# Optimization experiments

Hardware: AMD Instinct MI355X
Metric: run time of the kernel (lower is better)

## Reference

```python
import jax, jax.numpy as jnp
import numpy as np

C = 1152            # hidden_size
HEADS_LA = 36       # LiteLA heads = hidden_size // 32
HEADS_X = 16        # cross-attention heads
HID = int(C * 2.5)  # GLUMBConv hidden = 2880
B, N, M = 2, 4096, 300
EPS_LA = 1e-8
EPS_LN = 1e-6


def _ln(x):
    # LayerNorm without affine (adaLN-single style)
    mu = jnp.mean(x, -1, keepdims=True)
    var = jnp.mean((x - mu) ** 2, -1, keepdims=True)
    return (x - mu) * jax.lax.rsqrt(var + EPS_LN)


def _lite_la(x, qkv_w, proj_w, proj_b):
    b, n, c = x.shape
    d = c // HEADS_LA
    qkv = x @ qkv_w.T                       # (B,N,3C)
    q, k, v = jnp.split(qkv, 3, -1)
    r = lambda t: t.transpose(0, 2, 1).reshape(b, HEADS_LA, d, n)
    q = jax.nn.relu(r(q))
    k = jax.nn.relu(r(k))
    v = r(v)
    # pad v with a row of ones (PAD_VAL=1) for the normalizer
    v = jnp.concatenate([v, jnp.ones((b, HEADS_LA, 1, n), v.dtype)], 2)  # (B,h,d+1,N)
    vk = jnp.einsum('bhdn,bhen->bhde', v, k)    # (B,h,d+1,d)
    out = jnp.einsum('bhde,bhen->bhdn', vk, q)  # (B,h,d+1,N)
    out = out[:, :, :-1] / (out[:, :, -1:] + EPS_LA)
    out = out.reshape(b, c, n).transpose(0, 2, 1)
    return out @ proj_w.T + proj_b


def _cross(x, y, q_w, q_b, kv_w, kv_b, pw, pb):
    b, n, c = x.shape
    d = c // HEADS_X
    q = (x @ q_w.T + q_b).reshape(b, n, HEADS_X, d).transpose(0, 2, 1, 3)
    k, v = jnp.split(y @ kv_w.T + kv_b, 2, -1)
    k = k.reshape(b, -1, HEADS_X, d).transpose(0, 2, 1, 3)
    v = v.reshape(b, -1, HEADS_X, d).transpose(0, 2, 1, 3)
    scale = float(1.0 / np.sqrt(d))
    a = jax.nn.softmax(jnp.einsum('bhnd,bhmd->bhnm', q, k) * scale, -1)
    o = jnp.einsum('bhnm,bhmd->bhnd', a, v).transpose(0, 2, 1, 3).reshape(b, n, c)
    return o @ pw.T + pb


def _glumb(x, inv_w, inv_b, dw_w, dw_b, pw_w):
    b, n, c = x.shape
    H = W = int(np.sqrt(n))
    h = jax.nn.silu(x @ inv_w.T + inv_b)          # 1x1 inverted conv + silu, (B,N,2*HID)
    h = h.transpose(0, 2, 1).reshape(b, 2 * HID, H, W)
    h = jax.lax.conv_general_dilated(
        h, dw_w, (1, 1), 'SAME',
        feature_group_count=2 * HID,
        dimension_numbers=('NCHW', 'OIHW', 'NCHW'))
    h = h + dw_b[None, :, None, None]
    a, g = jnp.split(h, 2, 1)
    h = a * jax.nn.silu(g)                         # GLU
    h = h.reshape(b, HID, n).transpose(0, 2, 1)
    return h @ pw_w.T                              # 1x1 point conv, no bias/act


def setup_inputs() -> dict:
    key = jax.random.key(0)
    ks = jax.random.split(key, 12)
    p = lambda k, shp: (0.02 * jax.random.normal(k, shp)).astype(jnp.float32)
    z = lambda shp: jnp.zeros(shp, jnp.float32)
    return dict(
        x=jax.random.normal(ks[0], (B, N, C), jnp.float32),
        y=jax.random.normal(ks[1], (B, M, C), jnp.float32),
        t=jax.random.normal(ks[2], (B, 6, C), jnp.float32),
        sst=p(ks[3], (6, C)),
        qkv_w=p(ks[4], (3 * C, C)),
        aproj_w=p(ks[5], (C, C)), aproj_b=z((C,)),
        q_w=p(ks[6], (C, C)), q_b=z((C,)),
        kv_w=p(ks[7], (2 * C, C)), kv_b=z((2 * C,)),
        cproj_w=p(ks[8], (C, C)), cproj_b=z((C,)),
        inv_w=p(ks[9], (2 * HID, C)), inv_b=z((2 * HID,)),
        dw_w=p(ks[10], (2 * HID, 1, 3, 3)), dw_b=z((2 * HID,)),
        pw_w=p(ks[11], (C, HID)),
    )


def reference(x, y, t, sst, qkv_w, aproj_w, aproj_b, q_w, q_b, kv_w, kv_b,
              cproj_w, cproj_b, inv_w, inv_b, dw_w, dw_b, pw_w):
    m = sst[None] + t  # (B,6,C)
    sh_a, sc_a, g_a, sh_m, sc_m, g_m = [m[:, i:i + 1] for i in range(6)]
    x = x + g_a * _lite_la(_ln(x) * (1 + sc_a) + sh_a, qkv_w, aproj_w, aproj_b)
    x = x + _cross(x, y, q_w, q_b, kv_w, kv_b, cproj_w, cproj_b)
    x = x + g_m * _glumb(_ln(x) * (1 + sc_m) + sh_m, inv_w, inv_b, dw_w, dw_b, pw_w)
    return x
```

## Files before the change

### kernel.cpp

```cpp
#include <hip/hip_runtime.h>
#include <hip/hip_bf16.h>
#include <cstdint>
#include <cstddef>

#define CD    1152
#define NTOK  4096
#define MTOK  300
#define BSZ   2
#define HID2  5760
#define HIDD  2880
#define ROWS  (BSZ*NTOK)
#define KVROWS (BSZ*MTOK)

using bf16 = __hip_bfloat16;
typedef __bf16 bf16x8 __attribute__((ext_vector_type(8)));
typedef float f32x4 __attribute__((ext_vector_type(4)));

__device__ __forceinline__ float b2f(bf16 h) { return __bfloat162float(h); }
__device__ __forceinline__ bf16  f2b(float f) { return __float2bfloat16(f); }
__device__ __forceinline__ bf16x8 bz8() {
    bf16x8 v;
    #pragma unroll
    for (int j = 0; j < 8; ++j) v[j] = (__bf16)0.0f;
    return v;
}

__device__ __forceinline__ void gload16(const void* g, void* l) {
    __builtin_amdgcn_global_load_lds(
        (const __attribute__((address_space(1))) void*)g,
        (__attribute__((address_space(3))) void*)l, 16, 0, 0);
}

__global__ void cast_bf(const float* __restrict__ in, bf16* __restrict__ o, int n) {
    int i = blockIdx.x * 256 + threadIdx.x;
    if (i < n) o[i] = f2b(in[i]);
}

__global__ void zero_f32(float* __restrict__ p, int n) {
    int i = blockIdx.x * 256 + threadIdx.x;
    if (i < n) p[i] = 0.f;
}

__global__ void add_mod(const float* __restrict__ sst, const float* __restrict__ t,
                        float* __restrict__ m, int n, int per) {
    int i = blockIdx.x * 256 + threadIdx.x;
    if (i < n) m[i] = sst[i % per] + t[i];
}

__global__ void prep_dww(const float* __restrict__ dww, bf16* __restrict__ wt) {
    int i = blockIdx.x * 256 + threadIdx.x;
    if (i < 9 * HID2) {
        const int k = i / HID2, c = i - k * HID2;
        wt[i] = f2b(dww[c * 9 + k]);
    }
}

__global__ __launch_bounds__(256) void ln_mod(
    const float* __restrict__ xf, const float* __restrict__ m,
    int shRow, int scRow, bf16* __restrict__ out) {
    const int row = blockIdx.x;
    const int b = row >> 12;
    float s = 0.f, s2 = 0.f;
    for (int c = threadIdx.x; c < CD; c += 256) {
        float v = xf[(size_t)row * CD + c];
        s += v; s2 += v * v;
    }
    #pragma unroll
    for (int off = 32; off; off >>= 1) {
        s  += __shfl_down(s,  off, 64);
        s2 += __shfl_down(s2, off, 64);
    }
    __shared__ float red[8];
    const int wid = threadIdx.x >> 6, lane = threadIdx.x & 63;
    if (lane == 0) { red[wid] = s; red[4 + wid] = s2; }
    __syncthreads();
    s  = red[0] + red[1] + red[2] + red[3];
    s2 = red[4] + red[5] + red[6] + red[7];
    const float mu  = s / CD;
    const float var = s2 / CD - mu * mu;
    const float rs  = rsqrtf(var + 1e-6f);
    const float* sh = &m[((size_t)b * 6 + shRow) * CD];
    const float* sc = &m[((size_t)b * 6 + scRow) * CD];
    for (int c = threadIdx.x; c < CD; c += 256) {
        float v = xf[(size_t)row * CD + c];
        out[(size_t)row * CD + c] = f2b((v - mu) * rs * (1.f + sc[c]) + sh[c]);
    }
}

template<int EPI>
__global__ __launch_bounds__(256) void gemm_bt(
    const bf16* __restrict__ A, const bf16* __restrict__ W,
    const float* __restrict__ bias, const float* __restrict__ resf,
    const float* __restrict__ gate, int gateStride,
    bf16* __restrict__ outb, float* __restrict__ outf,
    int rows, int K, int Nout, int reluCols) {
    __shared__ __align__(16) char smem[33792];
    bf16* As = (bf16*)smem;
    bf16* Bs = (bf16*)(smem + 16384);
    const int tid = threadIdx.x;
    const int row0 = blockIdx.x * 128;
    const int col0 = blockIdx.y * 128;
    const int wid = tid >> 6, lane = tid & 63;
    const int wm = wid & 1, wn = wid >> 1;
    const int l16 = lane & 15, l4 = lane >> 4;
    f32x4 acc[4][4] = {};

    const int sr = tid >> 3;
    const int kbsw = (((tid & 7) ^ (sr & 7)) << 3);
    int gra[4], gcl[4];
    #pragma unroll
    for (int p = 0; p < 4; ++p) {
        int r = row0 + p * 32 + sr; if (r >= rows) r = rows - 1;
        gra[p] = r;
        gcl[p] = col0 + p * 32 + sr;
    }
    char* AsB = smem + wid * 1024;
    char* BsB = smem + 16384 + wid * 1024;

    for (int k0 = 0; k0 < K; k0 += 64) {
        __syncthreads();
        #pragma unroll
        for (int p = 0; p < 4; ++p) {
            gload16(&A[(size_t)gra[p] * K + k0 + kbsw], AsB + p * 4096);
            gload16(&W[(size_t)gcl[p] * K + k0 + kbsw], BsB + p * 4096);
        }
        __syncthreads();
        #pragma unroll
        for (int kk = 0; kk < 2; ++kk) {
            bf16x8 a[4], b[4];
            #pragma unroll
            for (int i = 0; i < 4; ++i) {
                const int ar = wm * 64 + i * 16 + l16;
                a[i] = *(const bf16x8*)&As[ar * 64 + ((((kk << 2) + l4) ^ (ar & 7)) << 3)];
            }
            #pragma unroll
            for (int j = 0; j < 4; ++j) {
                const int br = wn * 64 + j * 16 + l16;
                b[j] = *(const bf16x8*)&Bs[br * 64 + ((((kk << 2) + l4) ^ (br & 7)) << 3)];
            }
            #pragma unroll
            for (int i = 0; i < 4; ++i)
                #pragma unroll
                for (int j = 0; j < 4; ++j)
                    acc[i][j] = __builtin_amdgcn_mfma_f32_16x16x32_bf16(a[i], b[j], acc[i][j], 0, 0, 0);
        }
    }

    float* Lf = (float*)smem;
    const int erow = tid >> 4;
    const int ecol = (tid & 15) * 8;
    const int gc = col0 + ecol;
    #pragma unroll
    for (int pass = 0; pass < 2; ++pass) {
        __syncthreads();
        if (wm == pass) {
            #pragma unroll
            for (int i = 0; i < 4; ++i)
                #pragma unroll
                for (int j = 0; j < 4; ++j) {
                    const int lc = wn * 64 + j * 16 + l16;
                    #pragma unroll
                    for (int r = 0; r < 4; ++r)
                        Lf[(i * 16 + l4 * 4 + r) * 130 + lc] = acc[i][j][r];
                }
        }
        __syncthreads();
        #pragma unroll
        for (int rr = 0; rr < 4; ++rr) {
            const int lrow = rr * 16 + erow;
            const int gr = row0 + pass * 64 + lrow;
            if (gr >= rows) continue;
            float v[8];
            #pragma unroll
            for (int c = 0; c < 8; ++c) v[c] = Lf[lrow * 130 + ecol + c];
            const size_t oi0 = (size_t)gr * Nout + gc;
            if (EPI == 0) {
                bf16x8 ob;
                #pragma unroll
                for (int c = 0; c < 8; ++c) ob[c] = (__bf16)(v[c] + bias[gc + c]);
                *(bf16x8*)&outb[oi0] = ob;
            } else if (EPI == 1) {
                bf16x8 ob;
                #pragma unroll
                for (int c = 0; c < 8; ++c) {
                    float t = v[c];
                    if (gc + c < reluCols) t = fmaxf(t, 0.0f);
                    ob[c] = (__bf16)t;
                }
                *(bf16x8*)&outb[oi0] = ob;
            } else if (EPI == 2) {
                bf16x8 ob;
                #pragma unroll
                for (int c = 0; c < 8; ++c) {
                    float t = v[c] + bias[gc + c];
                    t = t / (1.0f + __expf(-t));
                    ob[c] = (__bf16)t;
                }
                *(bf16x8*)&outb[oi0] = ob;
            } else if (EPI == 3) {
                const float* gp = &gate[(gr >> 12) * gateStride + gc];
                const float* rp = &resf[oi0];
                f32x4 o0, o1; bf16x8 ob;
                #pragma unroll
                for (int c = 0; c < 8; ++c) {
                    float t = v[c] + bias[gc + c];
                    t = rp[c] + gp[c] * t;
                    if (c < 4) o0[c] = t; else o1[c - 4] = t;
                    ob[c] = (__bf16)t;
                }
                *(f32x4*)&outf[oi0] = o0;
                *(f32x4*)&outf[oi0 + 4] = o1;
                *(bf16x8*)&outb[oi0] = ob;
            } else if (EPI == 4) {
                const float* rp = &resf[oi0];
                f32x4 o0, o1;
                #pragma unroll
                for (int c = 0; c < 8; ++c) {
                    float t = rp[c] + v[c] + bias[gc + c];
                    if (c < 4) o0[c] = t; else o1[c - 4] = t;
                }
                *(f32x4*)&outf[oi0] = o0;
                *(f32x4*)&outf[oi0 + 4] = o1;
            } else {
                const float* gp = &gate[(gr >> 12) * gateStride + gc];
                const float* rp = &resf[oi0];
                f32x4 o0, o1;
                #pragma unroll
                for (int c = 0; c < 8; ++c) {
                    float t = rp[c] + gp[c] * v[c];
                    if (c < 4) o0[c] = t; else o1[c - 4] = t;
                }
                *(f32x4*)&outf[oi0] = o0;
                *(f32x4*)&outf[oi0 + 4] = o1;
            }
        }
    }
}

__global__ __launch_bounds__(256) void lite_vk(
    const bf16* __restrict__ qkv, float* __restrict__ vk) {
    const int b = blockIdx.x / 36, h = blockIdx.x % 36;
    const int n0 = blockIdx.y * 256;
    __shared__ bf16 ksm[64 * 32];
    __shared__ bf16 vsm[64 * 32];
    const int t = threadIdx.x;
    const int ev = t >> 3, kq = (t & 7) * 4;
    float a0 = 0, a1 = 0, a2 = 0, a3 = 0;
    float q0 = 0, q1 = 0, q2 = 0, q3 = 0;
    for (int tile = 0; tile < 4; ++tile) {
        const int nb = n0 + tile * 64;
        __syncthreads();
        {
            const int nl = t >> 2, part = (t & 3) * 8;
            const size_t rbase = ((size_t)b * NTOK + nb + nl) * (3 * CD);
            *(bf16x8*)&ksm[nl * 32 + part] = *(const bf16x8*)&qkv[rbase + CD     + h * 32 + part];
            *(bf16x8*)&vsm[nl * 32 + part] = *(const bf16x8*)&qkv[rbase + 2 * CD + h * 32 + part];
        }
        __syncthreads();
        #pragma unroll 4
        for (int nl = 0; nl < 64; ++nl) {
            const float vv = b2f(vsm[nl * 32 + ev]);
            const float k0 = b2f(ksm[nl * 32 + kq + 0]);
            const float k1 = b2f(ksm[nl * 32 + kq + 1]);
            const float k2 = b2f(ksm[nl * 32 + kq + 2]);
            const float k3 = b2f(ksm[nl * 32 + kq + 3]);
            a0 += vv * k0; a1 += vv * k1; a2 += vv * k2; a3 += vv * k3;
            if (ev == 0) { q0 += k0; q1 += k1; q2 += k2; q3 += k3; }
        }
    }
    float* dst = &vk[(((size_t)b * 36 + h) * 33 + ev) * 32 + kq];
    atomicAdd(dst + 0, a0); atomicAdd(dst + 1, a1);
    atomicAdd(dst + 2, a2); atomicAdd(dst + 3, a3);
    if (ev == 0) {
        float* d2 = &vk[(((size_t)b * 36 + h) * 33 + 32) * 32 + kq];
        atomicAdd(d2 + 0, q0); atomicAdd(d2 + 1, q1);
        atomicAdd(d2 + 2, q2); atomicAdd(d2 + 3, q3);
    }
}

__global__ __launch_bounds__(256) void lite_out(
    const bf16* __restrict__ qkv, const float* __restrict__ vk,
    bf16* __restrict__ u) {
    const int b = blockIdx.x / 36, h = blockIdx.x % 36;
    const int n = blockIdx.y * 256 + threadIdx.x;
    __shared__ float vks[33 * 32];
    const float* src = &vk[((size_t)b * 36 + h) * 33 * 32];
    for (int i = threadIdx.x; i < 33 * 32; i += 256) vks[i] = src[i];
    __syncthreads();
    float q[32];
    const bf16* qp = &qkv[((size_t)b * NTOK + n) * (3 * CD) + h * 32];
    #pragma unroll
    for (int e = 0; e < 32; ++e) q[e] = b2f(qp[e]);
    float denom = 0.f;
    #pragma unroll
    for (int e = 0; e < 32; ++e) denom += vks[32 * 32 + e] * q[e];
    const float rd = 1.f / (denom + 1e-8f);
    bf16* up = &u[((size_t)b * NTOK + n) * CD + h * 32];
    #pragma unroll 1
    for (int d = 0; d < 32; ++d) {
        float acc = 0.f;
        #pragma unroll
        for (int e = 0; e < 32; ++e) acc += vks[d * 32 + e] * q[e];
        up[d] = f2b(acc * rd);
    }
}

__global__ __launch_bounds__(256) void cross_attn_mfma(
    const bf16* __restrict__ qx, const bf16* __restrict__ kvb,
    bf16* __restrict__ attn) {
    const int b = blockIdx.x >> 4, h = blockIdx.x & 15;
    const int row0 = blockIdx.y * 64;
    __shared__ bf16 Ks[320 * 72];
    __shared__ bf16 Vt[80 * 328];
    __shared__ bf16 Ps[64 * 328];
    const int tid = threadIdx.x;
    const int wid = tid >> 6, lane = tid & 63;
    const int l16 = lane & 15, l4 = lane >> 4;
    const bf16 zb = f2b(0.f);
    const bf16x8 zv8 = bz8();

    for (int i = tid; i < 80 * 328; i += 256) Vt[i] = zb;
    for (int idx = tid; idx < 320 * 9; idx += 256) {
        const int m = idx / 9, part = (idx % 9) * 8;
        if (m < MTOK)
            *(bf16x8*)&Ks[m * 72 + part] =
                *(const bf16x8*)&kvb[((size_t)b * MTOK + m) * (2 * CD) + h * 72 + part];
        else
            *(bf16x8*)&Ks[m * 72 + part] = zv8;
    }
    __syncthreads();
    for (int i = tid; i < MTOK * 72; i += 256) {
        const int m = i / 72, d = i - m * 72;
        Vt[d * 328 + m] = kvb[((size_t)b * MTOK + m) * (2 * CD) + CD + h * 72 + d];
    }
    for (int i = lane; i < 16 * 16; i += 64)
        Ps[(wid * 16 + (i >> 4)) * 328 + 304 + (i & 15)] = zb;

    bf16x8 aq[3];
    {
        const int qrow = row0 + wid * 16 + l16;
        const bf16* qp = &qx[((size_t)b * NTOK + qrow) * CD + h * 72];
        aq[0] = *(const bf16x8*)&qp[l4 * 8];
        aq[1] = *(const bf16x8*)&qp[32 + l4 * 8];
        aq[2] = (l4 == 0) ? *(const bf16x8*)&qp[64] : zv8;
    }

    f32x4 sa[19] = {};
    #pragma unroll
    for (int t = 0; t < 19; ++t) {
        const bf16* kr = &Ks[(t * 16 + l16) * 72];
        bf16x8 b0 = *(const bf16x8*)&kr[l4 * 8];
        bf16x8 b1 = *(const bf16x8*)&kr[32 + l4 * 8];
        bf16x8 b2 = (l4 == 0) ? *(const bf16x8*)&kr[64] : zv8;
        sa[t] = __builtin_amdgcn_mfma_f32_16x16x32_bf16(aq[0], b0, sa[t], 0, 0, 0);
        sa[t] = __builtin_amdgcn_mfma_f32_16x16x32_bf16(aq[1], b1, sa[t], 0, 0, 0);
        sa[t] = __builtin_amdgcn_mfma_f32_16x16x32_bf16(aq[2], b2, sa[t], 0, 0, 0);
    }

    const float scale = 0.11785113019775792f;
    if (l16 >= 12) { sa[18][0] = sa[18][1] = sa[18][2] = sa[18][3] = -3.0e37f; }
    float mr[4] = {-3.0e38f, -3.0e38f, -3.0e38f, -3.0e38f};
    #pragma unroll
    for (int t = 0; t < 19; ++t)
        #pragma unroll
        for (int r = 0; r < 4; ++r) {
            const float s = sa[t][r] * scale;
            sa[t][r] = s;
            mr[r] = fmaxf(mr[r], s);
        }
    #pragma unroll
    for (int off = 1; off < 16; off <<= 1)
        #pragma unroll
        for (int r = 0; r < 4; ++r)
            mr[r] = fmaxf(mr[r], __shfl_xor(mr[r], off, 64));
    float lr[4] = {0.f, 0.f, 0.f, 0.f};
    #pragma unroll
    for (int t = 0; t < 19; ++t)
        #pragma unroll
        for (int r = 0; r < 4; ++r) {
            const float p = __expf(sa[t][r] - mr[r]);
            lr[r] += p;
            Ps[(wid * 16 + l4 * 4 + r) * 328 + t * 16 + l16] = f2b(p);
        }
    #pragma unroll
    for (int off = 1; off < 16; off <<= 1)
        #pragma unroll
        for (int r = 0; r < 4; ++r)
            lr[r] += __shfl_xor(lr[r], off, 64);
    __syncthreads();

    f32x4 oa[5] = {};
    #pragma unroll
    for (int kc = 0; kc < 10; ++kc) {
        bf16x8 pa = *(const bf16x8*)&Ps[(wid * 16 + l16) * 328 + kc * 32 + l4 * 8];
        #pragma unroll
        for (int dt = 0; dt < 5; ++dt) {
            bf16x8 vb = *(const bf16x8*)&Vt[(dt * 16 + l16) * 328 + kc * 32 + l4 * 8];
            oa[dt] = __builtin_amdgcn_mfma_f32_16x16x32_bf16(pa, vb, oa[dt], 0, 0, 0);
        }
    }
    #pragma unroll
    for (int r = 0; r < 4; ++r) {
        const float rinv = 1.f / lr[r];
        const int gr = row0 + wid * 16 + l4 * 4 + r;
        bf16* op = &attn[((size_t)b * NTOK + gr) * CD + h * 72];
        #pragma unroll
        for (int dt = 0; dt < 5; ++dt) {
            const int d = dt * 16 + l16;
            if (d < 72) op[d] = f2b(oa[dt][r] * rinv);
        }
    }
}

__global__ __launch_bounds__(128) void dwconv_glu2(
    const bf16* __restrict__ hbuf, const bf16* __restrict__ wt,
    const float* __restrict__ dwb, bf16* __restrict__ glu) {
    const int cg = blockIdx.y * 128 + threadIdx.x;
    if (cg >= 360) return;
    const int c0 = cg * 8;
    const int n = blockIdx.x & 4095;
    const int b = blockIdx.x >> 12;
    const int y0 = n >> 6, x0 = n & 63;
    float a[8], g[8];
    #pragma unroll
    for (int j = 0; j < 8; ++j) { a[j] = dwb[c0 + j]; g[j] = dwb[HIDD + c0 + j]; }
    #pragma unroll
    for (int dy = -1; dy <= 1; ++dy) {
        const int yy = y0 + dy;
        if (yy < 0 || yy >= 64) continue;
        #pragma unroll
        for (int dx = -1; dx <= 1; ++dx) {
            const int xx = x0 + dx;
            if (xx < 0 || xx >= 64) continue;
            const int k = (dy + 1) * 3 + (dx + 1);
            const size_t base = ((size_t)b * NTOK + yy * 64 + xx) * HID2;
            const bf16x8 va = *(const bf16x8*)&hbuf[base + c0];
            const bf16x8 vg = *(const bf16x8*)&hbuf[base + HIDD + c0];
            const bf16x8 wa = *(const bf16x8*)&wt[k * HID2 + c0];
            const bf16x8 wg = *(const bf16x8*)&wt[k * HID2 + HIDD + c0];
            #pragma unroll
            for (int j = 0; j < 8; ++j) {
                a[j] += (float)wa[j] * (float)va[j];
                g[j] += (float)wg[j] * (float)vg[j];
            }
        }
    }
    bf16x8 o;
    #pragma unroll
    for (int j = 0; j < 8; ++j) {
        const float s = g[j] / (1.f + __expf(-g[j]));
        o[j] = (__bf16)(a[j] * s);
    }
    *(bf16x8*)&glu[((size_t)b * NTOK + n) * HIDD + c0] = o;
}

extern "C" void kernel_launch(void* const* d_in, const int* in_sizes, int n_in,
                              void* d_out, int out_size, void* d_ws, size_t ws_size,
                              hipStream_t stream) {
    (void)in_sizes; (void)n_in; (void)out_size; (void)ws_size;
    const float* x       = (const float*)d_in[0];
    const float* y       = (const float*)d_in[1];
    const float* t       = (const float*)d_in[2];
    const float* sst     = (const float*)d_in[3];
    const float* qkv_w   = (const float*)d_in[4];
    const float* aproj_w = (const float*)d_in[5];
    const float* aproj_b = (const float*)d_in[6];
    const float* q_w     = (const float*)d_in[7];
    const float* q_b     = (const float*)d_in[8];
    const float* kv_w    = (const float*)d_in[9];
    const float* kv_b    = (const float*)d_in[10];
    const float* cproj_w = (const float*)d_in[11];
    const float* cproj_b = (const float*)d_in[12];
    const float* inv_w   = (const float*)d_in[13];
    const float* inv_b   = (const float*)d_in[14];
    const float* dw_w    = (const float*)d_in[15];
    const float* dw_b    = (const float*)d_in[16];
    const float* pw_w    = (const float*)d_in[17];
    float* out = (float*)d_out;

    char* ws = (char*)d_ws;
    size_t cur = 0;
    auto take = [&](size_t bytes) -> char* {
        char* p = ws + cur;
        cur = (cur + bytes + 255) & ~(size_t)255;
        return p;
    };
    float* mbuf   = (float*)take(BSZ * 6 * CD * 4);
    float* vkbuf  = (float*)take(BSZ * 36 * 33 * 32 * 4);
    bf16* wqkv    = (bf16*)take((size_t)3 * CD * CD * 2);
    bf16* waproj  = (bf16*)take((size_t)CD * CD * 2);
    bf16* wq      = (bf16*)take((size_t)CD * CD * 2);
    bf16* wkv     = (bf16*)take((size_t)2 * CD * CD * 2);
    bf16* wcproj  = (bf16*)take((size_t)CD * CD * 2);
    bf16* winv    = (bf16*)take((size_t)HID2 * CD * 2);
    bf16* wpw     = (bf16*)take((size_t)CD * HIDD * 2);
    bf16* wtdw    = (bf16*)take((size_t)9 * HID2 * 2);
    bf16* yb      = (bf16*)take((size_t)KVROWS * CD * 2);
    bf16* kvbuf   = (bf16*)take((size_t)KVROWS * 2 * CD * 2);
    bf16* P       = (bf16*)take((size_t)ROWS * HID2 * 2);
    bf16* Q       = (bf16*)take((size_t)ROWS * HIDD * 2);
    bf16* R       = (bf16*)take((size_t)ROWS * CD * 2);
    bf16* S       = (bf16*)take((size_t)ROWS * CD * 2);
    float* xa_f   = (float*)take((size_t)ROWS * CD * 4);

    bf16* qkvb = P;  bf16* hbuf = P;
    bf16* ubuf = Q;  bf16* glub = Q;
    bf16* x1 = R, *xa_bf = R, *attnb = R, *x2 = R;
    bf16* qx = S;
    float* xb_f = out;

    auto cast = [&](const float* src, bf16* dst, int n) {
        cast_bf<<<(n + 255) / 256, 256, 0, stream>>>(src, dst, n);
    };

    add_mod<<<(BSZ * 6 * CD + 255) / 256, 256, 0, stream>>>(sst, t, mbuf, BSZ * 6 * CD, 6 * CD);
    cast(qkv_w,   wqkv,   3 * CD * CD);
    cast(aproj_w, waproj, CD * CD);
    cast(q_w,     wq,     CD * CD);
    cast(kv_w,    wkv,    2 * CD * CD);
    cast(cproj_w, wcproj, CD * CD);
    cast(inv_w,   winv,   HID2 * CD);
    cast(pw_w,    wpw,    CD * HIDD);
    cast(y,       yb,     KVROWS * CD);
    prep_dww<<<(9 * HID2 + 255) / 256, 256, 0, stream>>>(dw_w, wtdw);

    ln_mod<<<ROWS, 256, 0, stream>>>(x, mbuf, 0, 1, x1);
    gemm_bt<1><<<dim3(64, 27), 256, 0, stream>>>(x1, wqkv, nullptr, nullptr, nullptr, 0,
                                                 qkvb, nullptr, ROWS, CD, 3 * CD, 2 * CD);
    zero_f32<<<(BSZ * 36 * 33 * 32 + 255) / 256, 256, 0, stream>>>(vkbuf, BSZ * 36 * 33 * 32);
    lite_vk<<<dim3(72, 16), 256, 0, stream>>>(qkvb, vkbuf);
    lite_out<<<dim3(72, 16), 256, 0, stream>>>(qkvb, vkbuf, ubuf);
    gemm_bt<3><<<dim3(64, 9), 256, 0, stream>>>(ubuf, waproj, aproj_b, x, mbuf + 2 * CD, 6 * CD,
                                                xa_bf, xa_f, ROWS, CD, CD, 0);

    gemm_bt<0><<<dim3(64, 9), 256, 0, stream>>>(xa_bf, wq, q_b, nullptr, nullptr, 0,
                                                qx, nullptr, ROWS, CD, CD, 0);
    gemm_bt<0><<<dim3(5, 18), 256, 0, stream>>>(yb, wkv, kv_b, nullptr, nullptr, 0,
                                                kvbuf, nullptr, KVROWS, CD, 2 * CD, 0);
    cross_attn_mfma<<<dim3(32, 64), 256, 0, stream>>>(qx, kvbuf, attnb);
    gemm_bt<4><<<dim3(64, 9), 256, 0, stream>>>(attnb, wcproj, cproj_b, xa_f, nullptr, 0,
                                                nullptr, xb_f, ROWS, CD, CD, 0);

    ln_mod<<<ROWS, 256, 0, stream>>>(xb_f, mbuf, 3, 4, x2);
    gemm_bt<2><<<dim3(64, 45), 256, 0, stream>>>(x2, winv, inv_b, nullptr, nullptr, 0,
                                                 hbuf, nullptr, ROWS, CD, HID2, 0);
    dwconv_glu2<<<dim3(ROWS, 3), 128, 0, stream>>>(hbuf, wtdw, dw_b, glub);
    gemm_bt<5><<<dim3(64, 9), 256, 0, stream>>>(glub, wpw, nullptr, xb_f, mbuf + 5 * CD, 6 * CD,
                                                nullptr, out, ROWS, HIDD, CD, 0);
}
```

Baseline: 1.185 ms.

## Fuse prep kernels, vectorize LN, remap GEMM blocks per XCD, pre-layout cross-attn K/V

All weight casts, the modulation add, the depthwise-weight transpose and the vk zeroing are merged into one vectorized prep kernel, replacing many small launches. LayerNorm loads x once into registers as float4 and writes bf16x4, avoiding a second read. GEMM blocks use a 1D grid remapped so that row tiles sharing A are grouped on the same XCD for L2 reuse. Cross-attention K and transposed V are built once per (batch, head) in global memory and copied into LDS with vector loads, instead of every block redoing the scalar transpose.

```diff
diff --git a/kernel.cpp b/kernel.cpp
--- a/kernel.cpp
+++ b/kernel.cpp
@@ -14,6 +14,7 @@
 
 using bf16 = __hip_bfloat16;
 typedef __bf16 bf16x8 __attribute__((ext_vector_type(8)));
+typedef __bf16 bf16x4 __attribute__((ext_vector_type(4)));
 typedef float f32x4 __attribute__((ext_vector_type(4)));
 
 __device__ __forceinline__ float b2f(bf16 h) { return __bfloat162float(h); }
@@ -31,39 +32,88 @@
         (__attribute__((address_space(3))) void*)l, 16, 0, 0);
 }
 
-__global__ void cast_bf(const float* __restrict__ in, bf16* __restrict__ o, int n) {
-    int i = blockIdx.x * 256 + threadIdx.x;
-    if (i < n) o[i] = f2b(in[i]);
-}
-
-__global__ void zero_f32(float* __restrict__ p, int n) {
-    int i = blockIdx.x * 256 + threadIdx.x;
-    if (i < n) p[i] = 0.f;
-}
-
-__global__ void add_mod(const float* __restrict__ sst, const float* __restrict__ t,
-                        float* __restrict__ m, int n, int per) {
-    int i = blockIdx.x * 256 + threadIdx.x;
-    if (i < n) m[i] = sst[i % per] + t[i];
-}
-
-__global__ void prep_dww(const float* __restrict__ dww, bf16* __restrict__ wt) {
-    int i = blockIdx.x * 256 + threadIdx.x;
-    if (i < 9 * HID2) {
+#define PB0 497664
+#define PB1 663552
+#define PB2 829440
+#define PB3 1161216
+#define PB4 1327104
+#define PB5 2156544
+#define PB6 2571264
+#define PB7 2657664
+#define PB8 2659392
+#define PB9 2665872
+#define PB10 2675376
+
+__device__ __forceinline__ void cast8(const float* __restrict__ s, bf16* __restrict__ d, int i) {
+    f32x4 a = *(const f32x4*)&s[i];
+    f32x4 b = *(const f32x4*)&s[i + 4];
+    bf16x8 o;
+    #pragma unroll
+    for (int j = 0; j < 4; ++j) { o[j] = (__bf16)a[j]; o[4 + j] = (__bf16)b[j]; }
+    *(bf16x8*)&d[i] = o;
+}
+
+__global__ __launch_bounds__(256) void prep_all(
+    const float* __restrict__ qkv_w, const float* __restrict__ aproj_w,
+    const float* __restrict__ q_w, const float* __restrict__ kv_w,
+    const float* __restrict__ cproj_w, const float* __restrict__ inv_w,
+    const float* __restrict__ pw_w, const float* __restrict__ y,
+    const float* __restrict__ sst, const float* __restrict__ tt,
+    const float* __restrict__ dww,
+    bf16* __restrict__ wqkv, bf16* __restrict__ waproj, bf16* __restrict__ wq,
+    bf16* __restrict__ wkv, bf16* __restrict__ wcproj, bf16* __restrict__ winv,
+    bf16* __restrict__ wpw, bf16* __restrict__ yb, float* __restrict__ mbuf,
+    bf16* __restrict__ wtdw, float* __restrict__ vkbuf) {
+    const int u = blockIdx.x * 256 + threadIdx.x;
+    if (u < PB0)      cast8(qkv_w,   wqkv,   u * 8);
+    else if (u < PB1) cast8(aproj_w, waproj, (u - PB0) * 8);
+    else if (u < PB2) cast8(q_w,     wq,     (u - PB1) * 8);
+    else if (u < PB3) cast8(kv_w,    wkv,    (u - PB2) * 8);
+    else if (u < PB4) cast8(cproj_w, wcproj, (u - PB3) * 8);
+    else if (u < PB5) cast8(inv_w,   winv,   (u - PB4) * 8);
+    else if (u < PB6) cast8(pw_w,    wpw,    (u - PB5) * 8);
+    else if (u < PB7) cast8(y,       yb,     (u - PB6) * 8);
+    else if (u < PB8) {
+        const int i = (u - PB7) * 8;
+        const int si = (i < 6 * CD) ? i : i - 6 * CD;
+        #pragma unroll
+        for (int c = 0; c < 2; ++c) {
+            f32x4 a = *(const f32x4*)&tt[i + c * 4];
+            f32x4 s = *(const f32x4*)&sst[si + c * 4];
+            f32x4 o;
+            #pragma unroll
+            for (int j = 0; j < 4; ++j) o[j] = a[j] + s[j];
+            *(f32x4*)&mbuf[i + c * 4] = o;
+        }
+    } else if (u < PB9) {
+        const int i = (u - PB8) * 8;
         const int k = i / HID2, c = i - k * HID2;
-        wt[i] = f2b(dww[c * 9 + k]);
+        bf16x8 o;
+        #pragma unroll
+        for (int j = 0; j < 8; ++j) o[j] = (__bf16)dww[(c + j) * 9 + k];
+        *(bf16x8*)&wtdw[i] = o;
+    } else if (u < PB10) {
+        const int i = (u - PB9) * 8;
+        f32x4 z = {};
+        *(f32x4*)&vkbuf[i] = z;
+        *(f32x4*)&vkbuf[i + 4] = z;
     }
 }
 
 __global__ __launch_bounds__(256) void ln_mod(
     const float* __restrict__ xf, const float* __restrict__ m,
     int shRow, int scRow, bf16* __restrict__ out) {
-    const int row = blockIdx.x;
+    const int row = blockIdx.x, tid = threadIdx.x;
     const int b = row >> 12;
+    const f32x4* xr = (const f32x4*)(xf + (size_t)row * CD);
+    f32x4 v0 = xr[tid];
+    f32x4 v1 = {};
+    if (tid < 32) v1 = xr[256 + tid];
     float s = 0.f, s2 = 0.f;
-    for (int c = threadIdx.x; c < CD; c += 256) {
-        float v = xf[(size_t)row * CD + c];
-        s += v; s2 += v * v;
+    #pragma unroll
+    for (int j = 0; j < 4; ++j) {
+        s += v0[j] + v1[j];
+        s2 += v0[j] * v0[j] + v1[j] * v1[j];
     }
     #pragma unroll
     for (int off = 32; off; off >>= 1) {
@@ -71,7 +121,7 @@
         s2 += __shfl_down(s2, off, 64);
     }
     __shared__ float red[8];
-    const int wid = threadIdx.x >> 6, lane = threadIdx.x & 63;
+    const int wid = tid >> 6, lane = tid & 63;
     if (lane == 0) { red[wid] = s; red[4 + wid] = s2; }
     __syncthreads();
     s  = red[0] + red[1] + red[2] + red[3];
@@ -79,11 +129,22 @@
     const float mu  = s / CD;
     const float var = s2 / CD - mu * mu;
     const float rs  = rsqrtf(var + 1e-6f);
-    const float* sh = &m[((size_t)b * 6 + shRow) * CD];
-    const float* sc = &m[((size_t)b * 6 + scRow) * CD];
-    for (int c = threadIdx.x; c < CD; c += 256) {
-        float v = xf[(size_t)row * CD + c];
-        out[(size_t)row * CD + c] = f2b((v - mu) * rs * (1.f + sc[c]) + sh[c]);
+    const f32x4* shp = (const f32x4*)&m[((size_t)b * 6 + shRow) * CD];
+    const f32x4* scp = (const f32x4*)&m[((size_t)b * 6 + scRow) * CD];
+    bf16x4* ob = (bf16x4*)(out + (size_t)row * CD);
+    {
+        f32x4 sh = shp[tid], sc = scp[tid];
+        bf16x4 o;
+        #pragma unroll
+        for (int j = 0; j < 4; ++j) o[j] = (__bf16)((v0[j] - mu) * rs * (1.f + sc[j]) + sh[j]);
+        ob[tid] = o;
+    }
+    if (tid < 32) {
+        f32x4 sh = shp[256 + tid], sc = scp[256 + tid];
+        bf16x4 o;
+        #pragma unroll
+        for (int j = 0; j < 4; ++j) o[j] = (__bf16)((v1[j] - mu) * rs * (1.f + sc[j]) + sh[j]);
+        ob[256 + tid] = o;
     }
 }
 
@@ -93,13 +154,22 @@
     const float* __restrict__ bias, const float* __restrict__ resf,
     const float* __restrict__ gate, int gateStride,
     bf16* __restrict__ outb, float* __restrict__ outf,
-    int rows, int K, int Nout, int reluCols) {
+    int rows, int K, int Nout, int reluCols, int nRowB, int nColB) {
     __shared__ __align__(16) char smem[33792];
     bf16* As = (bf16*)smem;
     bf16* Bs = (bf16*)(smem + 16384);
+    const int bid = blockIdx.x;
+    int row_blk, col_blk;
+    if ((nRowB & 7) == 0) {
+        const int rpx = nRowB >> 3;
+        const int xcd = bid & 7;
+        const int i = bid >> 3;
+        row_blk = xcd * rpx + (i % rpx);
+        col_blk = i / rpx;
+    } else { row_blk = bid % nRowB; col_blk = bid / nRowB; }
+    const int row0 = row_blk * 128;
+    const int col0 = col_blk * 128;
     const int tid = threadIdx.x;
-    const int row0 = blockIdx.x * 128;
-    const int col0 = blockIdx.y * 128;
     const int wid = tid >> 6, lane = tid & 63;
     const int wm = wid & 1, wn = wid >> 1;
     const int l16 = lane & 15, l4 = lane >> 4;
@@ -289,8 +359,13 @@
     __syncthreads();
     float q[32];
     const bf16* qp = &qkv[((size_t)b * NTOK + n) * (3 * CD) + h * 32];
-    #pragma unroll
-    for (int e = 0; e < 32; ++e) q[e] = b2f(qp[e]);
+    const bf16x8* qv = (const bf16x8*)qp;
+    #pragma unroll
+    for (int w = 0; w < 4; ++w) {
+        bf16x8 qq = qv[w];
+        #pragma unroll
+        for (int e = 0; e < 8; ++e) q[w * 8 + e] = (float)qq[e];
+    }
     float denom = 0.f;
     #pragma unroll
     for (int e = 0; e < 32; ++e) denom += vks[32 * 32 + e] * q[e];
@@ -305,10 +380,34 @@
     }
 }
 
+__global__ __launch_bounds__(256) void prep_attn(
+    const bf16* __restrict__ kvb, bf16* __restrict__ Kp, bf16* __restrict__ VtG) {
+    const int b = blockIdx.x >> 4, h = blockIdx.x & 15;
+    const int tid = threadIdx.x;
+    bf16* kp = Kp + (size_t)blockIdx.x * (320 * 72);
+    bf16* vt = VtG + (size_t)blockIdx.x * (80 * 328);
+    const bf16x8 z = bz8();
+    for (int i = tid; i < 320 * 9; i += 256) {
+        const int m = i / 9, part = (i % 9) * 8;
+        bf16x8 v = z;
+        if (m < MTOK)
+            v = *(const bf16x8*)&kvb[((size_t)b * MTOK + m) * (2 * CD) + h * 72 + part];
+        *(bf16x8*)&kp[m * 72 + part] = v;
+    }
+    for (int i = tid; i < 80 * 328; i += 256) {
+        const int d = i / 328, mm = i - d * 328;
+        bf16 v = f2b(0.f);
+        if (mm < MTOK && d < 72)
+            v = kvb[((size_t)b * MTOK + mm) * (2 * CD) + CD + h * 72 + d];
+        vt[i] = v;
+    }
+}
+
 __global__ __launch_bounds__(256) void cross_attn_mfma(
-    const bf16* __restrict__ qx, const bf16* __restrict__ kvb,
-    bf16* __restrict__ attn) {
-    const int b = blockIdx.x >> 4, h = blockIdx.x & 15;
+    const bf16* __restrict__ qx, const bf16* __restrict__ Kp,
+    const bf16* __restrict__ VtG, bf16* __restrict__ attn) {
+    const int bh = blockIdx.x;
+    const int b = bh >> 4;
     const int row0 = blockIdx.y * 64;
     __shared__ bf16 Ks[320 * 72];
     __shared__ bf16 Vt[80 * 328];
@@ -319,19 +418,13 @@
     const bf16 zb = f2b(0.f);
     const bf16x8 zv8 = bz8();
 
-    for (int i = tid; i < 80 * 328; i += 256) Vt[i] = zb;
-    for (int idx = tid; idx < 320 * 9; idx += 256) {
-        const int m = idx / 9, part = (idx % 9) * 8;
-        if (m < MTOK)
-            *(bf16x8*)&Ks[m * 72 + part] =
-                *(const bf16x8*)&kvb[((size_t)b * MTOK + m) * (2 * CD) + h * 72 + part];
-        else
-            *(bf16x8*)&Ks[m * 72 + part] = zv8;
-    }
-    __syncthreads();
-    for (int i = tid; i < MTOK * 72; i += 256) {
-        const int m = i / 72, d = i - m * 72;
-        Vt[d * 328 + m] = kvb[((size_t)b * MTOK + m) * (2 * CD) + CD + h * 72 + d];
+    {
+        const bf16x8* Kg = (const bf16x8*)(Kp + (size_t)bh * (320 * 72));
+        bf16x8* Kl = (bf16x8*)Ks;
+        for (int i = tid; i < 2880; i += 256) Kl[i] = Kg[i];
+        const bf16x8* Vg = (const bf16x8*)(VtG + (size_t)bh * (80 * 328));
+        bf16x8* Vl = (bf16x8*)Vt;
+        for (int i = tid; i < 3280; i += 256) Vl[i] = Vg[i];
     }
     for (int i = lane; i < 16 * 16; i += 64)
         Ps[(wid * 16 + (i >> 4)) * 328 + 304 + (i & 15)] = zb;
@@ -339,11 +432,12 @@
     bf16x8 aq[3];
     {
         const int qrow = row0 + wid * 16 + l16;
-        const bf16* qp = &qx[((size_t)b * NTOK + qrow) * CD + h * 72];
+        const bf16* qp = &qx[((size_t)b * NTOK + qrow) * CD + (bh & 15) * 72];
         aq[0] = *(const bf16x8*)&qp[l4 * 8];
         aq[1] = *(const bf16x8*)&qp[32 + l4 * 8];
         aq[2] = (l4 == 0) ? *(const bf16x8*)&qp[64] : zv8;
     }
+    __syncthreads();
 
     f32x4 sa[19] = {};
     #pragma unroll
@@ -403,7 +497,7 @@
     for (int r = 0; r < 4; ++r) {
         const float rinv = 1.f / lr[r];
         const int gr = row0 + wid * 16 + l4 * 4 + r;
-        bf16* op = &attn[((size_t)b * NTOK + gr) * CD + h * 72];
+        bf16* op = &attn[((size_t)b * NTOK + gr) * CD + (bh & 15) * 72];
         #pragma unroll
         for (int dt = 0; dt < 5; ++dt) {
             const int d = dt * 16 + l16;
@@ -497,6 +591,8 @@
     bf16* wtdw    = (bf16*)take((size_t)9 * HID2 * 2);
     bf16* yb      = (bf16*)take((size_t)KVROWS * CD * 2);
     bf16* kvbuf   = (bf16*)take((size_t)KVROWS * 2 * CD * 2);
+    bf16* Kp      = (bf16*)take((size_t)32 * 320 * 72 * 2);
+    bf16* VtG     = (bf16*)take((size_t)32 * 80 * 328 * 2);
     bf16* P       = (bf16*)take((size_t)ROWS * HID2 * 2);
     bf16* Q       = (bf16*)take((size_t)ROWS * HIDD * 2);
     bf16* R       = (bf16*)take((size_t)ROWS * CD * 2);
@@ -509,42 +605,31 @@
     bf16* qx = S;
     float* xb_f = out;
 
-    auto cast = [&](const float* src, bf16* dst, int n) {
-        cast_bf<<<(n + 255) / 256, 256, 0, stream>>>(src, dst, n);
-    };
-
-    add_mod<<<(BSZ * 6 * CD + 255) / 256, 256, 0, stream>>>(sst, t, mbuf, BSZ * 6 * CD, 6 * CD);
-    cast(qkv_w,   wqkv,   3 * CD * CD);
-    cast(aproj_w, waproj, CD * CD);
-    cast(q_w,     wq,     CD * CD);
-    cast(kv_w,    wkv,    2 * CD * CD);
-    cast(cproj_w, wcproj, CD * CD);
-    cast(inv_w,   winv,   HID2 * CD);
-    cast(pw_w,    wpw,    CD * HIDD);
-    cast(y,       yb,     KVROWS * CD);
-    prep_dww<<<(9 * HID2 + 255) / 256, 256, 0, stream>>>(dw_w, wtdw);
+    prep_all<<<(PB10 + 255) / 256, 256, 0, stream>>>(
+        qkv_w, aproj_w, q_w, kv_w, cproj_w, inv_w, pw_w, y, sst, t, dw_w,
+        wqkv, waproj, wq, wkv, wcproj, winv, wpw, yb, mbuf, wtdw, vkbuf);
 
     ln_mod<<<ROWS, 256, 0, stream>>>(x, mbuf, 0, 1, x1);
-    gemm_bt<1><<<dim3(64, 27), 256, 0, stream>>>(x1, wqkv, nullptr, nullptr, nullptr, 0,
-                                                 qkvb, nullptr, ROWS, CD, 3 * CD, 2 * CD);
-    zero_f32<<<(BSZ * 36 * 33 * 32 + 255) / 256, 256, 0, stream>>>(vkbuf, BSZ * 36 * 33 * 32);
+    gemm_bt<1><<<64 * 27, 256, 0, stream>>>(x1, wqkv, nullptr, nullptr, nullptr, 0,
+                                            qkvb, nullptr, ROWS, CD, 3 * CD, 2 * CD, 64, 27);
     lite_vk<<<dim3(72, 16), 256, 0, stream>>>(qkvb, vkbuf);
     lite_out<<<dim3(72, 16), 256, 0, stream>>>(qkvb, vkbuf, ubuf);
-    gemm_bt<3><<<dim3(64, 9), 256, 0, stream>>>(ubuf, waproj, aproj_b, x, mbuf + 2 * CD, 6 * CD,
-                                                xa_bf, xa_f, ROWS, CD, CD, 0);
-
-    gemm_bt<0><<<dim3(64, 9), 256, 0, stream>>>(xa_bf, wq, q_b, nullptr, nullptr, 0,
-                                                qx, nullptr, ROWS, CD, CD, 0);
-    gemm_bt<0><<<dim3(5, 18), 256, 0, stream>>>(yb, wkv, kv_b, nullptr, nullptr, 0,
-                                                kvbuf, nullptr, KVROWS, CD, 2 * CD, 0);
-    cross_attn_mfma<<<dim3(32, 64), 256, 0, stream>>>(qx, kvbuf, attnb);
-    gemm_bt<4><<<dim3(64, 9), 256, 0, stream>>>(attnb, wcproj, cproj_b, xa_f, nullptr, 0,
-                                                nullptr, xb_f, ROWS, CD, CD, 0);
+    gemm_bt<3><<<64 * 9, 256, 0, stream>>>(ubuf, waproj, aproj_b, x, mbuf + 2 * CD, 6 * CD,
+                                           xa_bf, xa_f, ROWS, CD, CD, 0, 64, 9);
+
+    gemm_bt<0><<<64 * 9, 256, 0, stream>>>(xa_bf, wq, q_b, nullptr, nullptr, 0,
+                                           qx, nullptr, ROWS, CD, CD, 0, 64, 9);
+    gemm_bt<0><<<5 * 18, 256, 0, stream>>>(yb, wkv, kv_b, nullptr, nullptr, 0,
+                                           kvbuf, nullptr, KVROWS, CD, 2 * CD, 0, 5, 18);
+    prep_attn<<<32, 256, 0, stream>>>(kvbuf, Kp, VtG);
+    cross_attn_mfma<<<dim3(32, 64), 256, 0, stream>>>(qx, Kp, VtG, attnb);
+    gemm_bt<4><<<64 * 9, 256, 0, stream>>>(attnb, wcproj, cproj_b, xa_f, nullptr, 0,
+                                           nullptr, xb_f, ROWS, CD, CD, 0, 64, 9);
 
     ln_mod<<<ROWS, 256, 0, stream>>>(xb_f, mbuf, 3, 4, x2);
-    gemm_bt<2><<<dim3(64, 45), 256, 0, stream>>>(x2, winv, inv_b, nullptr, nullptr, 0,
-                                                 hbuf, nullptr, ROWS, CD, HID2, 0);
+    gemm_bt<2><<<64 * 45, 256, 0, stream>>>(x2, winv, inv_b, nullptr, nullptr, 0,
+                                            hbuf, nullptr, ROWS, CD, HID2, 0, 64, 45);
     dwconv_glu2<<<dim3(ROWS, 3), 128, 0, stream>>>(hbuf, wtdw, dw_b, glub);
-    gemm_bt<5><<<dim3(64, 9), 256, 0, stream>>>(glub, wpw, nullptr, xb_f, mbuf + 5 * CD, 6 * CD,
-                                                nullptr, out, ROWS, HIDD, CD, 0);
-}
+    gemm_bt<5><<<64 * 9, 256, 0, stream>>>(glub, wpw, nullptr, xb_f, mbuf + 5 * CD, 6 * CD,
+                                           nullptr, out, ROWS, HIDD, CD, 0, 64, 9);
+}
```

After: 1.106 ms. 6.7% less time.
